# Kernel optimization log

Measured on AMD Instinct MI355X. Metric: run time of the kernel, lower is better.

Reference implementation:

```python
import jax, jax.numpy as jnp
import numpy as np

B, T, C = 8, 8192, 512

def setup_inputs() -> dict:
    key = jax.random.key(0)
    x = jax.random.normal(key, (B, T, C), dtype=jnp.float32)
    return {"x": x}

def reference(x) -> jnp.ndarray:
    # Causal bag-of-words: out[b, t] = mean(x[b, :t+1]).
    # Equivalent to softmax over zero logits with a causal mask, then matmul,
    # but computed as an O(T*C) cumulative mean instead of an O(T^2*C) matmul.
    csum = jnp.cumsum(x, axis=1)                                  # (B, T, C)
    counts = jnp.arange(1, x.shape[1] + 1, dtype=x.dtype)[None, :, None]
    return csum / counts
```

## Files before the change

kernel.cpp:

```cpp
#include <hip/hip_runtime.h>


constexpr int B   = 8;
constexpr int T   = 8192;
constexpr int C   = 512;
constexpr int C4  = C / 4;
constexpr int L   = 64;
constexpr int NCH = T / L;

__device__ __forceinline__ float4 f4add(float4 a, float4 b) {
    return make_float4(a.x + b.x, a.y + b.y, a.z + b.z, a.w + b.w);
}

__global__ __launch_bounds__(256) void cbow_chunksums(
        const float4* __restrict__ x, float4* __restrict__ ws) {
    const int tid   = blockIdx.x * blockDim.x + threadIdx.x;
    const int c4    = tid & (C4 - 1);
    const int chunk = (tid / C4) & (NCH - 1);
    const int b     = tid / (C4 * NCH);

    const float4* p = x + ((b * T) + chunk * L) * C4 + c4;
    float4 s = make_float4(0.f, 0.f, 0.f, 0.f);
#pragma unroll 8
    for (int t = 0; t < L; ++t) {
        s = f4add(s, p[t * C4]);
    }
    ws[(b * NCH + chunk) * C4 + c4] = s;
}

__global__ __launch_bounds__(256) void cbow_scan(
        const float4* __restrict__ x, const float4* __restrict__ ws,
        float4* __restrict__ out) {
    const int tid   = blockIdx.x * blockDim.x + threadIdx.x;
    const int c4    = tid & (C4 - 1);
    const int chunk = (tid / C4) & (NCH - 1);
    const int b     = tid / (C4 * NCH);

    const float4* w = ws + b * NCH * C4 + c4;
    float4 run = make_float4(0.f, 0.f, 0.f, 0.f);
    for (int j = 0; j < chunk; ++j) {
        run = f4add(run, w[j * C4]);
    }

    const int   base = ((b * T) + chunk * L) * C4 + c4;
    const float4* p  = x + base;
    float4*       o  = out + base;
    const int     t0 = chunk * L;
#pragma unroll 4
    for (int t = 0; t < L; ++t) {
        run = f4add(run, p[t * C4]);
        const float inv = __builtin_amdgcn_rcpf((float)(t0 + t + 1));
        o[t * C4] = make_float4(run.x * inv, run.y * inv, run.z * inv, run.w * inv);
    }
}

extern "C" void kernel_launch(void* const* d_in, const int* in_sizes, int n_in,
                              void* d_out, int out_size, void* d_ws, size_t ws_size,
                              hipStream_t stream) {
    const float4* x   = (const float4*)d_in[0];
    float4*       out = (float4*)d_out;
    float4*       ws  = (float4*)d_ws;

    const int n_threads = B * NCH * C4;
    const int block = 256;
    const int grid  = n_threads / block;

    cbow_chunksums<<<grid, block, 0, stream>>>(x, ws);
    cbow_scan<<<grid, block, 0, stream>>>(x, ws, out);
}
```

Baseline: 259.6 us.

## Replace redundant per-thread chunk prefix sums with a dedicated exclusive scan kernel

```diff
diff --git a/kernel.cpp b/kernel.cpp
--- a/kernel.cpp
+++ b/kernel.cpp
@@ -1,70 +1,75 @@
 #include <hip/hip_runtime.h>
 
+
+typedef float v4f __attribute__((ext_vector_type(4)));
 
 constexpr int B   = 8;
 constexpr int T   = 8192;
 constexpr int C   = 512;
 constexpr int C4  = C / 4;
-constexpr int L   = 64;
+constexpr int L   = 32;
 constexpr int NCH = T / L;
+constexpr int NCOL = B * C4;
+constexpr int NTHREAD = B * NCH * C4;
 
-__device__ __forceinline__ float4 f4add(float4 a, float4 b) {
-    return make_float4(a.x + b.x, a.y + b.y, a.z + b.z, a.w + b.w);
-}
+__global__ __launch_bounds__(256, 4) void cbow_k1_chunksums(
+        const v4f* __restrict__ x, v4f* __restrict__ ws) {
+    const int tid   = blockIdx.x * 256 + threadIdx.x;
+    const int c4    = tid & (C4 - 1);
+    const int chunk = (tid >> 7) & (NCH - 1);
+    const int b     = tid >> 15;
 
-__global__ __launch_bounds__(256) void cbow_chunksums(
-        const float4* __restrict__ x, float4* __restrict__ ws) {
-    const int tid   = blockIdx.x * blockDim.x + threadIdx.x;
-    const int c4    = tid & (C4 - 1);
-    const int chunk = (tid / C4) & (NCH - 1);
-    const int b     = tid / (C4 * NCH);
-
-    const float4* p = x + ((b * T) + chunk * L) * C4 + c4;
-    float4 s = make_float4(0.f, 0.f, 0.f, 0.f);
-#pragma unroll 8
-    for (int t = 0; t < L; ++t) {
-        s = f4add(s, p[t * C4]);
-    }
+    const v4f* p = x + (size_t)(b * T + chunk * L) * C4 + c4;
+    v4f s = 0.f;
+#pragma unroll 16
+    for (int t = 0; t < L; ++t) s += p[t * C4];
     ws[(b * NCH + chunk) * C4 + c4] = s;
 }
 
-__global__ __launch_bounds__(256) void cbow_scan(
-        const float4* __restrict__ x, const float4* __restrict__ ws,
-        float4* __restrict__ out) {
-    const int tid   = blockIdx.x * blockDim.x + threadIdx.x;
+__global__ __launch_bounds__(256) void cbow_k2_scan(v4f* __restrict__ ws) {
+    const int col = blockIdx.x * 256 + threadIdx.x;
+    const int b   = col >> 7;
+    const int c4  = col & (C4 - 1);
+    v4f* w = ws + (size_t)b * NCH * C4 + c4;
+    v4f run = 0.f;
+#pragma unroll 8
+    for (int j = 0; j < NCH; ++j) {
+        v4f v = w[(size_t)j * C4];
+        w[(size_t)j * C4] = run;
+        run += v;
+    }
+}
+
+__global__ __launch_bounds__(256, 4) void cbow_k3_downsweep(
+        const v4f* __restrict__ x, const v4f* __restrict__ ws,
+        v4f* __restrict__ out) {
+    const int tid   = blockIdx.x * 256 + threadIdx.x;
     const int c4    = tid & (C4 - 1);
-    const int chunk = (tid / C4) & (NCH - 1);
-    const int b     = tid / (C4 * NCH);
+    const int chunk = (tid >> 7) & (NCH - 1);
+    const int b     = tid >> 15;
 
-    const float4* w = ws + b * NCH * C4 + c4;
-    float4 run = make_float4(0.f, 0.f, 0.f, 0.f);
-    for (int j = 0; j < chunk; ++j) {
-        run = f4add(run, w[j * C4]);
-    }
-
-    const int   base = ((b * T) + chunk * L) * C4 + c4;
-    const float4* p  = x + base;
-    float4*       o  = out + base;
-    const int     t0 = chunk * L;
-#pragma unroll 4
+    v4f run = ws[(b * NCH + chunk) * C4 + c4];
+    const int    t0   = chunk * L;
+    const size_t base = (size_t)(b * T + t0) * C4 + c4;
+    const v4f* p = x + base;
+    v4f*       o = out + base;
+#pragma unroll 16
     for (int t = 0; t < L; ++t) {
-        run = f4add(run, p[t * C4]);
+        run += p[t * C4];
         const float inv = __builtin_amdgcn_rcpf((float)(t0 + t + 1));
-        o[t * C4] = make_float4(run.x * inv, run.y * inv, run.z * inv, run.w * inv);
+        v4f r = run * inv;
+        __builtin_nontemporal_store(r, o + t * C4);
     }
 }
 
 extern "C" void kernel_launch(void* const* d_in, const int* in_sizes, int n_in,
                               void* d_out, int out_size, void* d_ws, size_t ws_size,
                               hipStream_t stream) {
-    const float4* x   = (const float4*)d_in[0];
-    float4*       out = (float4*)d_out;
-    float4*       ws  = (float4*)d_ws;
+    const v4f* x   = (const v4f*)d_in[0];
+    v4f*       out = (v4f*)d_out;
+    v4f*       ws  = (v4f*)d_ws;
 
-    const int n_threads = B * NCH * C4;
-    const int block = 256;
-    const int grid  = n_threads / block;
-
-    cbow_chunksums<<<grid, block, 0, stream>>>(x, ws);
-    cbow_scan<<<grid, block, 0, stream>>>(x, ws, out);
+    cbow_k1_chunksums<<<NTHREAD / 256, 256, 0, stream>>>(x, ws);
+    cbow_k2_scan<<<NCOL / 256, 256, 0, stream>>>(ws);
+    cbow_k3_downsweep<<<NTHREAD / 256, 256, 0, stream>>>(x, ws, out);
 }
```

Measured after the change: 269.2 us. 1.04x slower.

## Replace two-pass chunk scan with single-pass decoupled look-back scan

Applied to the files above, without the earlier changes.

```diff
diff --git a/kernel.cpp b/kernel.cpp
--- a/kernel.cpp
+++ b/kernel.cpp
@@ -1,70 +1,114 @@
 #include <hip/hip_runtime.h>
 
 
-constexpr int B   = 8;
-constexpr int T   = 8192;
-constexpr int C   = 512;
-constexpr int C4  = C / 4;
-constexpr int L   = 64;
+typedef float v4f __attribute__((ext_vector_type(4)));
+
+constexpr int B = 8, T = 8192, C4 = 128;
+constexpr int L = 32;
 constexpr int NCH = T / L;
+constexpr int NTILE = B * NCH;
+constexpr int RPT = 16;
 
-__device__ __forceinline__ float4 f4add(float4 a, float4 b) {
-    return make_float4(a.x + b.x, a.y + b.y, a.z + b.z, a.w + b.w);
+constexpr size_t FLAGS_OFF = 256;
+constexpr size_t AGG_OFF   = 16 * 1024;
+constexpr size_t INC_OFF   = AGG_OFF + (size_t)NTILE * C4 * sizeof(v4f);
+
+__global__ __launch_bounds__(256) void cbow_init(unsigned* ws) {
+    const int i = blockIdx.x * 256 + threadIdx.x;
+    if (i == 0) ws[0] = 0u;
+    unsigned* flags = ws + FLAGS_OFF / 4;
+    if (i < NTILE) flags[i] = 0u;
 }
 
-__global__ __launch_bounds__(256) void cbow_chunksums(
-        const float4* __restrict__ x, float4* __restrict__ ws) {
-    const int tid   = blockIdx.x * blockDim.x + threadIdx.x;
+__global__ __launch_bounds__(256) void cbow_scan_onepass(
+        const v4f* __restrict__ x, v4f* __restrict__ out,
+        unsigned char* __restrict__ wsb) {
+    unsigned* ticket = (unsigned*)wsb;
+    unsigned* flags  = (unsigned*)(wsb + FLAGS_OFF);
+    v4f* agg = (v4f*)(wsb + AGG_OFF);
+    v4f* inc = (v4f*)(wsb + INC_OFF);
+
+    __shared__ v4f s_sum[2][C4];
+    __shared__ v4f s_excl[C4];
+    __shared__ int s_tile;
+    __shared__ int s_state;
+
+    const int tid = threadIdx.x;
+    if (tid == 0) s_tile = (int)atomicAdd(ticket, 1u);
+    __syncthreads();
+    const int tile  = s_tile;
+    const int b     = tile >> 8;
+    const int chunk = tile & (NCH - 1);
     const int c4    = tid & (C4 - 1);
-    const int chunk = (tid / C4) & (NCH - 1);
-    const int b     = tid / (C4 * NCH);
+    const int h     = tid >> 7;
+    const int t0    = chunk * L + h * RPT;
 
-    const float4* p = x + ((b * T) + chunk * L) * C4 + c4;
-    float4 s = make_float4(0.f, 0.f, 0.f, 0.f);
-#pragma unroll 8
-    for (int t = 0; t < L; ++t) {
-        s = f4add(s, p[t * C4]);
-    }
-    ws[(b * NCH + chunk) * C4 + c4] = s;
-}
+    const v4f* p = x + (size_t)(b * T + t0) * C4 + c4;
+    v4f pref[RPT];
+    pref[0] = __builtin_nontemporal_load(p);
+#pragma unroll
+    for (int r = 1; r < RPT; ++r)
+        pref[r] = pref[r - 1] + __builtin_nontemporal_load(p + (size_t)r * C4);
 
-__global__ __launch_bounds__(256) void cbow_scan(
-        const float4* __restrict__ x, const float4* __restrict__ ws,
-        float4* __restrict__ out) {
-    const int tid   = blockIdx.x * blockDim.x + threadIdx.x;
-    const int c4    = tid & (C4 - 1);
-    const int chunk = (tid / C4) & (NCH - 1);
-    const int b     = tid / (C4 * NCH);
+    s_sum[h][c4] = pref[RPT - 1];
+    __syncthreads();
 
-    const float4* w = ws + b * NCH * C4 + c4;
-    float4 run = make_float4(0.f, 0.f, 0.f, 0.f);
-    for (int j = 0; j < chunk; ++j) {
-        run = f4add(run, w[j * C4]);
+    v4f aggv = s_sum[0][c4] + s_sum[1][c4];
+    if (chunk > 0) {
+        if (tid < C4) agg[(size_t)tile * C4 + c4] = aggv;
+        __syncthreads();
+        if (tid == 0) __atomic_store_n(&flags[tile], 1u, __ATOMIC_RELEASE);
     }
 
-    const int   base = ((b * T) + chunk * L) * C4 + c4;
-    const float4* p  = x + base;
-    float4*       o  = out + base;
-    const int     t0 = chunk * L;
-#pragma unroll 4
-    for (int t = 0; t < L; ++t) {
-        run = f4add(run, p[t * C4]);
-        const float inv = __builtin_amdgcn_rcpf((float)(t0 + t + 1));
-        o[t * C4] = make_float4(run.x * inv, run.y * inv, run.z * inv, run.w * inv);
+    v4f excl = 0.f;
+    if (chunk > 0) {
+        int j = tile - 1;
+        for (;;) {
+            if (tid == 0) {
+                unsigned f;
+                for (;;) {
+                    f = __atomic_load_n(&flags[j], __ATOMIC_RELAXED);
+                    if (f == 1u || f == 2u) break;
+                    __builtin_amdgcn_s_sleep(1);
+                }
+                __atomic_thread_fence(__ATOMIC_ACQUIRE);
+                s_state = (int)f;
+            }
+            __syncthreads();
+            const int st = s_state;
+            __syncthreads();
+            if (tid < C4) {
+                const v4f* pay = (st == 2) ? inc + (size_t)j * C4
+                                           : agg + (size_t)j * C4;
+                excl += pay[c4];
+            }
+            if (st == 2) break;
+            --j;
+        }
+    }
+
+    if (tid < C4) {
+        inc[(size_t)tile * C4 + c4] = excl + aggv;
+        s_excl[c4] = excl;
+    }
+    __syncthreads();
+    if (tid == 0) __atomic_store_n(&flags[tile], 2u, __ATOMIC_RELEASE);
+
+    const v4f base = s_excl[c4] + (h ? s_sum[0][c4] : (v4f)0.f);
+    v4f* o = out + (size_t)(b * T + t0) * C4 + c4;
+#pragma unroll
+    for (int r = 0; r < RPT; ++r) {
+        const float inv = __builtin_amdgcn_rcpf((float)(t0 + r + 1));
+        __builtin_nontemporal_store((base + pref[r]) * inv, o + (size_t)r * C4);
     }
 }
 
 extern "C" void kernel_launch(void* const* d_in, const int* in_sizes, int n_in,
                               void* d_out, int out_size, void* d_ws, size_t ws_size,
                               hipStream_t stream) {
-    const float4* x   = (const float4*)d_in[0];
-    float4*       out = (float4*)d_out;
-    float4*       ws  = (float4*)d_ws;
+    const v4f* x   = (const v4f*)d_in[0];
+    v4f*       out = (v4f*)d_out;
 
-    const int n_threads = B * NCH * C4;
-    const int block = 256;
-    const int grid  = n_threads / block;
-
-    cbow_chunksums<<<grid, block, 0, stream>>>(x, ws);
-    cbow_scan<<<grid, block, 0, stream>>>(x, ws, out);
+    cbow_init<<<NTILE / 256, 256, 0, stream>>>((unsigned*)d_ws);
+    cbow_scan_onepass<<<NTILE, 256, 0, stream>>>(x, out, (unsigned char*)d_ws);
 }
```

Measured after the change: 691.6 us. +166.4%, slower.
